# Optimization experiments

Measured on AMD Instinct MI355X. Metric: run time of the kernel, lower is better.

Reference implementation:

```python
import jax, jax.numpy as jnp
import numpy as np

VOCAB, H, HEADS, S, FF = 100, 8, 2, 6, 16
HD = H // HEADS  # head_dim = 4
EPS = 1e-5


def _layernorm(x, g, b):
    mu = jnp.mean(x, axis=-1, keepdims=True)
    var = jnp.mean((x - mu) ** 2, axis=-1, keepdims=True)
    return (x - mu) * jax.lax.rsqrt(var + EPS) * g + b


def setup_inputs() -> dict:
    key = jax.random.key(0)
    ks = jax.random.split(key, 20)
    B = 262144
    d = {
        'input_ids': jax.random.randint(ks[0], (B, S), 0, VOCAB),
        'tok_emb': jax.random.normal(ks[1], (VOCAB, H), jnp.float32) * 0.02,
        'pos_emb': jax.random.normal(ks[2], (S, H), jnp.float32) * 0.02,
        'Wq': jax.random.normal(ks[3], (H, H), jnp.float32) * 0.1,
        'bq': jnp.zeros((H,), jnp.float32),
        'Wk': jax.random.normal(ks[4], (H, H), jnp.float32) * 0.1,
        'bk': jnp.zeros((H,), jnp.float32),
        'Wv': jax.random.normal(ks[5], (H, H), jnp.float32) * 0.1,
        'bv': jnp.zeros((H,), jnp.float32),
        'Wo': jax.random.normal(ks[6], (H, H), jnp.float32) * 0.1,
        'bo': jnp.zeros((H,), jnp.float32),
        'W1': jax.random.normal(ks[7], (FF, H), jnp.float32) * 0.1,
        'b1': jnp.zeros((FF,), jnp.float32),
        'W2': jax.random.normal(ks[8], (H, FF), jnp.float32) * 0.1,
        'b2': jnp.zeros((H,), jnp.float32),
        'g1': jnp.ones((H,), jnp.float32),
        'be1': jnp.zeros((H,), jnp.float32),
        'g2': jnp.ones((H,), jnp.float32),
        'be2': jnp.zeros((H,), jnp.float32),
    }
    return d


def reference(input_ids, tok_emb, pos_emb, Wq, bq, Wk, bk, Wv, bv, Wo, bo,
              W1, b1, W2, b2, g1, be1, g2, be2):
    B, Sq = input_ids.shape
    x = tok_emb[input_ids] + pos_emb[None, :, :]  # [B,S,H]
    q = x @ Wq.T + bq
    k = x @ Wk.T + bk
    v = x @ Wv.T + bv
    # split heads: [B, heads, S, head_dim]
    q = q.reshape(B, Sq, HEADS, HD).transpose(0, 2, 1, 3)
    k = k.reshape(B, Sq, HEADS, HD).transpose(0, 2, 1, 3)
    v = v.reshape(B, Sq, HEADS, HD).transpose(0, 2, 1, 3)
    scores = jnp.einsum('bhsd,bhtd->bhst', q, k) / (HD ** 0.5)
    probs = jax.nn.softmax(scores, axis=-1)
    attn = jnp.einsum('bhst,bhtd->bhsd', probs, v)
    attn = attn.transpose(0, 2, 1, 3).reshape(B, Sq, H)
    attn = attn @ Wo.T + bo
    h = _layernorm(x + attn, g1, be1)
    ffn = jax.nn.gelu(h @ W1.T + b1, approximate=False) @ W2.T + b2
    return _layernorm(h + ffn, g2, be2)
```

## Files before the change

kernel.cpp:

```cpp
#include <hip/hip_runtime.h>

#define TT_S 6
#define TT_H 8
#define TT_FF 16
#define SEQ_PER_BLK 64
#define BLK (SEQ_PER_BLK * TT_S)
#define KV_STRIDE 108

__global__ __launch_bounds__(BLK, 6) void tt_fused(
    const int* __restrict__ ids,
    const float* __restrict__ tok_emb, const float* __restrict__ pos_emb,
    const float* __restrict__ Wq, const float* __restrict__ bq,
    const float* __restrict__ Wk, const float* __restrict__ bk,
    const float* __restrict__ Wv, const float* __restrict__ bv,
    const float* __restrict__ Wo, const float* __restrict__ bo,
    const float* __restrict__ W1, const float* __restrict__ b1,
    const float* __restrict__ W2, const float* __restrict__ b2,
    const float* __restrict__ g1, const float* __restrict__ be1,
    const float* __restrict__ g2, const float* __restrict__ be2,
    float* __restrict__ out, int B)
{
  __shared__ __align__(16) float s_tok[800];
  __shared__ __align__(16) float s_pos[48];
  __shared__ __align__(16) float s_kv[SEQ_PER_BLK * KV_STRIDE];

  const int tid = threadIdx.x;
  for (int i = tid; i < 800; i += BLK) s_tok[i] = tok_emb[i];
  if (tid < 48) s_pos[tid] = pos_emb[tid];
  __syncthreads();

  const int s_loc = tid / TT_S;
  const int t     = tid - s_loc * TT_S;
  const int seq_g = blockIdx.x * SEQ_PER_BLK + s_loc;
  const bool valid = (seq_g < B);

  const size_t gidx = (size_t)blockIdx.x * BLK + tid;
  const int id = valid ? ids[gidx] : 0;

  const float4* tr = (const float4*)(s_tok + id * TT_H);
  float4 a0 = tr[0];
  float4 a1 = tr[1];
  const float4* pr = (const float4*)(s_pos + t * TT_H);
  float4 p0 = pr[0];
  float4 p1 = pr[1];
  float xs[TT_H];
  xs[0] = a0.x + p0.x; xs[1] = a0.y + p0.y; xs[2] = a0.z + p0.z; xs[3] = a0.w + p0.w;
  xs[4] = a1.x + p1.x; xs[5] = a1.y + p1.y; xs[6] = a1.z + p1.z; xs[7] = a1.w + p1.w;

  {
    float kr[TT_H], vr[TT_H];
    #pragma unroll
    for (int i = 0; i < TT_H; ++i) {
      float ak = bk[i], av = bv[i];
      #pragma unroll
      for (int j = 0; j < TT_H; ++j) {
        ak = fmaf(xs[j], Wk[i*8+j], ak);
        av = fmaf(xs[j], Wv[i*8+j], av);
      }
      kr[i] = ak; vr[i] = av;
    }
    float* kvp = s_kv + s_loc * KV_STRIDE + t * 16;
    float4 w0; w0.x = kr[0]; w0.y = kr[1]; w0.z = kr[2]; w0.w = kr[3];
    float4 w1; w1.x = kr[4]; w1.y = kr[5]; w1.z = kr[6]; w1.w = kr[7];
    float4 w2; w2.x = vr[0]; w2.y = vr[1]; w2.z = vr[2]; w2.w = vr[3];
    float4 w3; w3.x = vr[4]; w3.y = vr[5]; w3.z = vr[6]; w3.w = vr[7];
    ((float4*)kvp)[0] = w0;
    ((float4*)kvp)[1] = w1;
    ((float4*)kvp)[2] = w2;
    ((float4*)kvp)[3] = w3;
  }
  __syncthreads();

  float qs[TT_H];
  #pragma unroll
  for (int i = 0; i < TT_H; ++i) {
    float a = bq[i];
    #pragma unroll
    for (int j = 0; j < TT_H; ++j) a = fmaf(xs[j], Wq[i*8+j], a);
    qs[i] = a * 0.5f;
  }

  float acc[TT_H] = {0.f,0.f,0.f,0.f,0.f,0.f,0.f,0.f};
  float sum0 = 0.f, sum1 = 0.f;
  const float4* kvb = (const float4*)(s_kv + s_loc * KV_STRIDE);
  #pragma unroll
  for (int t2 = 0; t2 < TT_S; ++t2) {
    float4 ka = kvb[t2*4+0];
    float4 kb = kvb[t2*4+1];
    float4 va = kvb[t2*4+2];
    float4 vb = kvb[t2*4+3];
    float d0 = qs[0]*ka.x;
    d0 = fmaf(qs[1], ka.y, d0);
    d0 = fmaf(qs[2], ka.z, d0);
    d0 = fmaf(qs[3], ka.w, d0);
    float d1 = qs[4]*kb.x;
    d1 = fmaf(qs[5], kb.y, d1);
    d1 = fmaf(qs[6], kb.z, d1);
    d1 = fmaf(qs[7], kb.w, d1);
    float e0 = __expf(d0);
    float e1 = __expf(d1);
    sum0 += e0; sum1 += e1;
    acc[0] = fmaf(e0, va.x, acc[0]);
    acc[1] = fmaf(e0, va.y, acc[1]);
    acc[2] = fmaf(e0, va.z, acc[2]);
    acc[3] = fmaf(e0, va.w, acc[3]);
    acc[4] = fmaf(e1, vb.x, acc[4]);
    acc[5] = fmaf(e1, vb.y, acc[5]);
    acc[6] = fmaf(e1, vb.z, acc[6]);
    acc[7] = fmaf(e1, vb.w, acc[7]);
  }
  {
    float inv0 = __builtin_amdgcn_rcpf(sum0);
    float inv1 = __builtin_amdgcn_rcpf(sum1);
    acc[0] *= inv0; acc[1] *= inv0; acc[2] *= inv0; acc[3] *= inv0;
    acc[4] *= inv1; acc[5] *= inv1; acc[6] *= inv1; acc[7] *= inv1;
  }

  float r[TT_H];
  float mu = 0.f;
  #pragma unroll
  for (int i = 0; i < TT_H; ++i) {
    float o = bo[i];
    #pragma unroll
    for (int j = 0; j < TT_H; ++j) o = fmaf(acc[j], Wo[i*8+j], o);
    r[i] = xs[i] + o;
    mu += r[i];
  }
  mu *= 0.125f;
  float var = 0.f;
  #pragma unroll
  for (int i = 0; i < TT_H; ++i) { float d = r[i] - mu; var = fmaf(d, d, var); }
  var *= 0.125f;
  float rin = __builtin_amdgcn_rsqf(var + 1e-5f);
  float hr[TT_H];
  #pragma unroll
  for (int i = 0; i < TT_H; ++i)
    hr[i] = fmaf((r[i] - mu) * rin, g1[i], be1[i]);

  float f1[TT_FF];
  #pragma unroll
  for (int f = 0; f < TT_FF; ++f) {
    float u = b1[f];
    #pragma unroll
    for (int j = 0; j < TT_H; ++j) u = fmaf(hr[j], W1[f*8+j], u);
    float u2 = u * u;
    float p  = fmaf(0.044715f, u2, 1.0f);
    float z2 = fminf(1.5957691216057308f * u * p, 60.f);
    float e  = __expf(z2);
    f1[f] = u * e * __builtin_amdgcn_rcpf(e + 1.0f);
  }

  float r2[TT_H];
  float mu2 = 0.f;
  #pragma unroll
  for (int i = 0; i < TT_H; ++i) {
    float y = b2[i];
    #pragma unroll
    for (int f = 0; f < TT_FF; ++f) y = fmaf(f1[f], W2[i*16+f], y);
    r2[i] = hr[i] + y;
    mu2 += r2[i];
  }
  mu2 *= 0.125f;
  float var2 = 0.f;
  #pragma unroll
  for (int i = 0; i < TT_H; ++i) { float d = r2[i] - mu2; var2 = fmaf(d, d, var2); }
  var2 *= 0.125f;
  float rin2 = __builtin_amdgcn_rsqf(var2 + 1e-5f);
  float res[TT_H];
  #pragma unroll
  for (int i = 0; i < TT_H; ++i)
    res[i] = fmaf((r2[i] - mu2) * rin2, g2[i], be2[i]);

  if (valid) {
    float* op = out + gidx * TT_H;
    float4 v0; v0.x = res[0]; v0.y = res[1]; v0.z = res[2]; v0.w = res[3];
    float4 v1; v1.x = res[4]; v1.y = res[5]; v1.z = res[6]; v1.w = res[7];
    ((float4*)op)[0] = v0;
    ((float4*)op)[1] = v1;
  }
}

extern "C" void kernel_launch(void* const* d_in, const int* in_sizes, int n_in,
                              void* d_out, int out_size, void* d_ws, size_t ws_size,
                              hipStream_t stream) {
  const int*   ids = (const int*)  d_in[0];
  const float* tok = (const float*)d_in[1];
  const float* pos = (const float*)d_in[2];
  const float* Wq  = (const float*)d_in[3];
  const float* bq  = (const float*)d_in[4];
  const float* Wk  = (const float*)d_in[5];
  const float* bk  = (const float*)d_in[6];
  const float* Wv  = (const float*)d_in[7];
  const float* bv  = (const float*)d_in[8];
  const float* Wo  = (const float*)d_in[9];
  const float* bo  = (const float*)d_in[10];
  const float* W1  = (const float*)d_in[11];
  const float* b1  = (const float*)d_in[12];
  const float* W2  = (const float*)d_in[13];
  const float* b2  = (const float*)d_in[14];
  const float* g1  = (const float*)d_in[15];
  const float* be1 = (const float*)d_in[16];
  const float* g2  = (const float*)d_in[17];
  const float* be2 = (const float*)d_in[18];
  float* out = (float*)d_out;

  const int B = in_sizes[0] / TT_S;
  const int grid = (B + SEQ_PER_BLK - 1) / SEQ_PER_BLK;
  hipLaunchKernelGGL(tt_fused, dim3(grid), dim3(BLK), 0, stream,
                     ids, tok, pos, Wq, bq, Wk, bk, Wv, bv, Wo, bo,
                     W1, b1, W2, b2, g1, be1, g2, be2, out, B);
}
```

Baseline: 142.8 us.

## Store K/V and token embeddings as packed fp16 in LDS, streamline softmax/GELU math

After: 142.5 us. About the same (-0.2%).

```diff
diff --git a/kernel.cpp b/kernel.cpp
--- a/kernel.cpp
+++ b/kernel.cpp
@@ -4,8 +4,16 @@
 #define TT_H 8
 #define TT_FF 16
 #define SEQ_PER_BLK 64
-#define BLK (SEQ_PER_BLK * TT_S)
-#define KV_STRIDE 108
+#define BLK 384
+#define KV_STRIDE_U 52
+
+typedef __fp16 h2_t __attribute__((ext_vector_type(2)));
+typedef __fp16 h8_t __attribute__((ext_vector_type(8)));
+
+__device__ __forceinline__ unsigned pk2(float a, float b) {
+  h2_t h = __builtin_amdgcn_cvt_pkrtz(a, b);
+  return __builtin_bit_cast(unsigned, h);
+}
 
 __global__ __launch_bounds__(BLK, 6) void tt_fused(
     const int* __restrict__ ids,
@@ -20,32 +28,32 @@
     const float* __restrict__ g2, const float* __restrict__ be2,
     float* __restrict__ out, int B)
 {
-  __shared__ __align__(16) float s_tok[800];
-  __shared__ __align__(16) float s_pos[48];
-  __shared__ __align__(16) float s_kv[SEQ_PER_BLK * KV_STRIDE];
+  __shared__ __align__(16) unsigned s_kv[SEQ_PER_BLK * KV_STRIDE_U];
+  __shared__ __align__(16) unsigned s_tok[400];
 
   const int tid = threadIdx.x;
-  for (int i = tid; i < 800; i += BLK) s_tok[i] = tok_emb[i];
-  if (tid < 48) s_pos[tid] = pos_emb[tid];
+  for (int i = tid; i < 400; i += BLK) {
+    float2 tv = ((const float2*)tok_emb)[i];
+    s_tok[i] = pk2(tv.x, tv.y);
+  }
   __syncthreads();
 
   const int s_loc = tid / TT_S;
   const int t     = tid - s_loc * TT_S;
   const int seq_g = blockIdx.x * SEQ_PER_BLK + s_loc;
   const bool valid = (seq_g < B);
-
   const size_t gidx = (size_t)blockIdx.x * BLK + tid;
   const int id = valid ? ids[gidx] : 0;
 
-  const float4* tr = (const float4*)(s_tok + id * TT_H);
-  float4 a0 = tr[0];
-  float4 a1 = tr[1];
-  const float4* pr = (const float4*)(s_pos + t * TT_H);
+  h8_t t0 = ((const h8_t*)s_tok)[id];
+  const float4* pr = (const float4*)(pos_emb + t * TT_H);
   float4 p0 = pr[0];
   float4 p1 = pr[1];
   float xs[TT_H];
-  xs[0] = a0.x + p0.x; xs[1] = a0.y + p0.y; xs[2] = a0.z + p0.z; xs[3] = a0.w + p0.w;
-  xs[4] = a1.x + p1.x; xs[5] = a1.y + p1.y; xs[6] = a1.z + p1.z; xs[7] = a1.w + p1.w;
+  xs[0] = (float)t0[0] + p0.x; xs[1] = (float)t0[1] + p0.y;
+  xs[2] = (float)t0[2] + p0.z; xs[3] = (float)t0[3] + p0.w;
+  xs[4] = (float)t0[4] + p1.x; xs[5] = (float)t0[5] + p1.y;
+  xs[6] = (float)t0[6] + p1.z; xs[7] = (float)t0[7] + p1.w;
 
   {
     float kr[TT_H], vr[TT_H];
@@ -59,15 +67,14 @@
       }
       kr[i] = ak; vr[i] = av;
     }
-    float* kvp = s_kv + s_loc * KV_STRIDE + t * 16;
-    float4 w0; w0.x = kr[0]; w0.y = kr[1]; w0.z = kr[2]; w0.w = kr[3];
-    float4 w1; w1.x = kr[4]; w1.y = kr[5]; w1.z = kr[6]; w1.w = kr[7];
-    float4 w2; w2.x = vr[0]; w2.y = vr[1]; w2.z = vr[2]; w2.w = vr[3];
-    float4 w3; w3.x = vr[4]; w3.y = vr[5]; w3.z = vr[6]; w3.w = vr[7];
-    ((float4*)kvp)[0] = w0;
-    ((float4*)kvp)[1] = w1;
-    ((float4*)kvp)[2] = w2;
-    ((float4*)kvp)[3] = w3;
+    unsigned* kvp = s_kv + s_loc * KV_STRIDE_U + t * 8;
+    uint4 w0, w1;
+    w0.x = pk2(kr[0], kr[1]); w0.y = pk2(kr[2], kr[3]);
+    w0.z = pk2(kr[4], kr[5]); w0.w = pk2(kr[6], kr[7]);
+    w1.x = pk2(vr[0], vr[1]); w1.y = pk2(vr[2], vr[3]);
+    w1.z = pk2(vr[4], vr[5]); w1.w = pk2(vr[6], vr[7]);
+    ((uint4*)kvp)[0] = w0;
+    ((uint4*)kvp)[1] = w1;
   }
   __syncthreads();
 
@@ -77,37 +84,35 @@
     float a = bq[i];
     #pragma unroll
     for (int j = 0; j < TT_H; ++j) a = fmaf(xs[j], Wq[i*8+j], a);
-    qs[i] = a * 0.5f;
+    qs[i] = a;
   }
 
   float acc[TT_H] = {0.f,0.f,0.f,0.f,0.f,0.f,0.f,0.f};
   float sum0 = 0.f, sum1 = 0.f;
-  const float4* kvb = (const float4*)(s_kv + s_loc * KV_STRIDE);
+  const h8_t* kvb = (const h8_t*)(s_kv + s_loc * KV_STRIDE_U);
   #pragma unroll
   for (int t2 = 0; t2 < TT_S; ++t2) {
-    float4 ka = kvb[t2*4+0];
-    float4 kb = kvb[t2*4+1];
-    float4 va = kvb[t2*4+2];
-    float4 vb = kvb[t2*4+3];
-    float d0 = qs[0]*ka.x;
-    d0 = fmaf(qs[1], ka.y, d0);
-    d0 = fmaf(qs[2], ka.z, d0);
-    d0 = fmaf(qs[3], ka.w, d0);
-    float d1 = qs[4]*kb.x;
-    d1 = fmaf(qs[5], kb.y, d1);
-    d1 = fmaf(qs[6], kb.z, d1);
-    d1 = fmaf(qs[7], kb.w, d1);
-    float e0 = __expf(d0);
-    float e1 = __expf(d1);
+    h8_t kh = kvb[t2*2];
+    h8_t vh = kvb[t2*2+1];
+    float d0 = (float)kh[0] * qs[0];
+    d0 = fmaf((float)kh[1], qs[1], d0);
+    d0 = fmaf((float)kh[2], qs[2], d0);
+    d0 = fmaf((float)kh[3], qs[3], d0);
+    float d1 = (float)kh[4] * qs[4];
+    d1 = fmaf((float)kh[5], qs[5], d1);
+    d1 = fmaf((float)kh[6], qs[6], d1);
+    d1 = fmaf((float)kh[7], qs[7], d1);
+    float e0 = __builtin_amdgcn_exp2f(d0 * 0.7213475204f);
+    float e1 = __builtin_amdgcn_exp2f(d1 * 0.7213475204f);
     sum0 += e0; sum1 += e1;
-    acc[0] = fmaf(e0, va.x, acc[0]);
-    acc[1] = fmaf(e0, va.y, acc[1]);
-    acc[2] = fmaf(e0, va.z, acc[2]);
-    acc[3] = fmaf(e0, va.w, acc[3]);
-    acc[4] = fmaf(e1, vb.x, acc[4]);
-    acc[5] = fmaf(e1, vb.y, acc[5]);
-    acc[6] = fmaf(e1, vb.z, acc[6]);
-    acc[7] = fmaf(e1, vb.w, acc[7]);
+    acc[0] = fmaf(e0, (float)vh[0], acc[0]);
+    acc[1] = fmaf(e0, (float)vh[1], acc[1]);
+    acc[2] = fmaf(e0, (float)vh[2], acc[2]);
+    acc[3] = fmaf(e0, (float)vh[3], acc[3]);
+    acc[4] = fmaf(e1, (float)vh[4], acc[4]);
+    acc[5] = fmaf(e1, (float)vh[5], acc[5]);
+    acc[6] = fmaf(e1, (float)vh[6], acc[6]);
+    acc[7] = fmaf(e1, (float)vh[7], acc[7]);
   }
   {
     float inv0 = __builtin_amdgcn_rcpf(sum0);
@@ -130,12 +135,12 @@
   float var = 0.f;
   #pragma unroll
   for (int i = 0; i < TT_H; ++i) { float d = r[i] - mu; var = fmaf(d, d, var); }
-  var *= 0.125f;
-  float rin = __builtin_amdgcn_rsqf(var + 1e-5f);
+  float rin = __builtin_amdgcn_rsqf(fmaf(var, 0.125f, 1e-5f));
+  float mc = mu * rin;
   float hr[TT_H];
   #pragma unroll
   for (int i = 0; i < TT_H; ++i)
-    hr[i] = fmaf((r[i] - mu) * rin, g1[i], be1[i]);
+    hr[i] = fmaf(fmaf(r[i], rin, -mc), g1[i], be1[i]);
 
   float f1[TT_FF];
   #pragma unroll
@@ -144,10 +149,9 @@
     #pragma unroll
     for (int j = 0; j < TT_H; ++j) u = fmaf(hr[j], W1[f*8+j], u);
     float u2 = u * u;
-    float p  = fmaf(0.044715f, u2, 1.0f);
-    float z2 = fminf(1.5957691216057308f * u * p, 60.f);
-    float e  = __expf(z2);
-    f1[f] = u * e * __builtin_amdgcn_rcpf(e + 1.0f);
+    float e  = __builtin_amdgcn_exp2f(u * fmaf(0.1029432f, u2, 2.3022072f));
+    float rr = __builtin_amdgcn_rcpf(e + 1.0f);
+    f1[f] = fmaf(-u, rr, u);
   }
 
   float r2[TT_H];
@@ -164,14 +168,14 @@
   float var2 = 0.f;
   #pragma unroll
   for (int i = 0; i < TT_H; ++i) { float d = r2[i] - mu2; var2 = fmaf(d, d, var2); }
-  var2 *= 0.125f;
-  float rin2 = __builtin_amdgcn_rsqf(var2 + 1e-5f);
-  float res[TT_H];
-  #pragma unroll
-  for (int i = 0; i < TT_H; ++i)
-    res[i] = fmaf((r2[i] - mu2) * rin2, g2[i], be2[i]);
+  float rin2 = __builtin_amdgcn_rsqf(fmaf(var2, 0.125f, 1e-5f));
+  float mc2 = mu2 * rin2;
 
   if (valid) {
+    float res[TT_H];
+    #pragma unroll
+    for (int i = 0; i < TT_H; ++i)
+      res[i] = fmaf(fmaf(r2[i], rin2, -mc2), g2[i], be2[i]);
     float* op = out + gidx * TT_H;
     float4 v0; v0.x = res[0]; v0.y = res[1]; v0.z = res[2]; v0.w = res[3];
     float4 v1; v1.x = res[4]; v1.y = res[5]; v1.z = res[6]; v1.w = res[7];
```
